# Optimization experiments

Hardware: AMD Instinct MI355X
Metric: run time of the kernel (lower is better)

The kernel has to match this reference:

```python
import jax, jax.numpy as jnp
import numpy as np

V, E, HID, L = 32000, 2048, 8192, 4
H, KV, DK, DH = 16, 4, 128, 128
SEQ, WINDOW = 2048, 1024
EPS = 1e-5


def rms_norm(x):
    return x * jax.lax.rsqrt(jnp.mean(x * x, axis=-1, keepdims=True) + EPS)


def rope_buffers(seq_len, key_size):
    half = key_size // 2
    offset = jnp.arange(key_size) % half
    scales = jnp.power(10000.0, -2.0 / key_size * offset.astype(jnp.float32))
    angles = jnp.arange(seq_len, dtype=jnp.float32)[:, None] * scales[None, :]  # [S, DK]
    cos = jnp.cos(angles)
    sin = jnp.sin(angles)
    sin = sin.at[:, :half].multiply(-1.0)
    return cos, sin


def rotate(f, cos, sin):
    # f: [B, heads, S, DK]; cos/sin: [S, DK]
    half = DK // 2
    swapped = jnp.concatenate([f[..., half:], f[..., :half]], axis=-1)
    return cos * f + sin * swapped


def sliding_window_attention(q, k, v, window):
    # q: [B,H,S,DK], k: [B,KV,S,DK], v: [B,KV,S,DH]; GQA broadcast
    B, _, S, _ = q.shape
    G = H // KV
    qg = q.reshape(B, KV, G, S, DK)
    scores = jnp.einsum('bkgqd,bkjd->bkgqj', qg, k) / jnp.sqrt(jnp.asarray(DK, q.dtype))
    i = jnp.arange(S)[:, None]
    j = jnp.arange(S)[None, :]
    mask = (j <= i) & (i - j < window)
    scores = jnp.where(mask, scores, jnp.asarray(-1e9, scores.dtype))
    probs = jax.nn.softmax(scores, axis=-1)
    out = jnp.einsum('bkgqj,bkjd->bkgqd', probs, v)
    return out.reshape(B, H, S, DH)


def setup_inputs() -> dict:
    key = jax.random.key(0)
    ks = jax.random.split(key, 9)
    s = lambda k, shape, fan: jax.random.normal(k, shape, jnp.float32) / np.sqrt(fan)
    return {
        'tokens': jax.random.randint(ks[0], (1, SEQ), 0, V),
        'table': jax.random.normal(ks[1], (V, E), jnp.float32) * 0.02,
        'wq': s(ks[2], (L, E, H * DK), E),
        'wk': s(ks[3], (L, E, KV * DK), E),
        'wv': s(ks[4], (L, E, KV * DH), E),
        'wo': s(ks[5], (L, H * DH, E), H * DH),
        'w_up': s(ks[6], (L, E, 2 * HID), E),
        'w_down': s(ks[7], (L, HID, E), HID),
        'w_vocab': s(ks[8], (E, V), E),
    }


def reference(tokens, table, wq, wk, wv, wo, w_up, w_down, w_vocab):
    B, S = tokens.shape
    table = table.at[0].set(0.0)  # forward zeroes row 0 each call
    cos, sin = rope_buffers(S, DK)
    x = table[tokens]  # [B, S, E]
    for l in range(L):
        # --- self attention ---
        n = rms_norm(x)
        q = (n @ wq[l]).reshape(B, S, H, DK).transpose(0, 2, 1, 3)
        k = (n @ wk[l]).reshape(B, S, KV, DK).transpose(0, 2, 1, 3)
        v = (n @ wv[l]).reshape(B, S, KV, DH).transpose(0, 2, 1, 3)
        q = rotate(q, cos, sin)
        k = rotate(k, cos, sin)
        attn = sliding_window_attention(q, k, v, WINDOW)
        attn = attn.transpose(0, 2, 1, 3).reshape(B, S, H * DH)
        x = x + attn @ wo[l]
        # --- SwiGLU FFN ---
        n = rms_norm(x)
        gu = n @ w_up[l]
        gate, up = gu[..., :HID], gu[..., HID:]
        x = x + (up * jax.nn.silu(gate)) @ w_down[l]
    x = rms_norm(x)
    logits = x @ w_vocab  # [B, S, V]
    return logits
```

## Files before the change

### kernel.cpp

```cpp
#include <hip/hip_runtime.h>
#include <cstdint>

typedef unsigned short bf16u;
typedef __attribute__((ext_vector_type(8))) short short8;
typedef __attribute__((ext_vector_type(4))) short short4v;
typedef __attribute__((ext_vector_type(4))) float f32x4;

#define SEQ   2048
#define EMB   2048
#define NHEAD 16
#define NKV   4
#define DKH   128
#define HIDN  8192
#define NVOC  32000
#define NLAY  4
#define WIN   1024
#define QKV_N 3072

__device__ __forceinline__ bf16u f2bf(float f) {
  union { float f; uint32_t u; } v; v.f = f;
  uint32_t r = v.u + 0x7FFFu + ((v.u >> 16) & 1u);
  return (bf16u)(r >> 16);
}

__device__ __forceinline__ void gl2lds16(const void* g, void* l) {
  __builtin_amdgcn_global_load_lds(
      (const __attribute__((address_space(1))) void*)g,
      (__attribute__((address_space(3))) void*)l, 16, 0, 0);
}

__global__ __launch_bounds__(256) void embed_kernel(const int* __restrict__ tokens,
                                                    const float* __restrict__ table,
                                                    float* __restrict__ x) {
  int s = blockIdx.x;
  int tok = tokens[s];
  int i0 = threadIdx.x * 8;
  float4 a = {0,0,0,0}, b = {0,0,0,0};
  if (tok != 0) {
    const float* src = table + (size_t)tok * EMB;
    a = *(const float4*)(src + i0);
    b = *(const float4*)(src + i0 + 4);
  }
  *(float4*)(x + (size_t)s * EMB + i0) = a;
  *(float4*)(x + (size_t)s * EMB + i0 + 4) = b;
}

__global__ __launch_bounds__(256) void rmsnorm_kernel(const float* __restrict__ x,
                                                      bf16u* __restrict__ out) {
  int s = blockIdx.x;
  const float* row = x + (size_t)s * EMB;
  int i0 = threadIdx.x * 8;
  float4 a = *(const float4*)(row + i0);
  float4 b = *(const float4*)(row + i0 + 4);
  float ss = a.x*a.x + a.y*a.y + a.z*a.z + a.w*a.w
           + b.x*b.x + b.y*b.y + b.z*b.z + b.w*b.w;
  #pragma unroll
  for (int off = 1; off < 64; off <<= 1) ss += __shfl_xor(ss, off);
  __shared__ float red[4];
  if ((threadIdx.x & 63) == 0) red[threadIdx.x >> 6] = ss;
  __syncthreads();
  float scale = rsqrtf((red[0] + red[1] + red[2] + red[3]) * (1.0f / EMB) + 1e-5f);
  float v[8] = {a.x, a.y, a.z, a.w, b.x, b.y, b.z, b.w};
  short8 o;
  #pragma unroll
  for (int j = 0; j < 8; ++j) o[j] = (short)f2bf(v[j] * scale);
  *(short8*)(out + (size_t)s * EMB + i0) = o;
}

__global__ __launch_bounds__(256) void reduce4norm_kernel(float* __restrict__ x,
                                                          const float* __restrict__ p,
                                                          bf16u* __restrict__ nout) {
  int s = blockIdx.x;
  const size_t MN = (size_t)SEQ * EMB;
  size_t base = (size_t)s * EMB + threadIdx.x * 8;
  float v[8];
  #pragma unroll
  for (int h = 0; h < 2; ++h) {
    size_t i = base + h * 4;
    float4 a  = *(const float4*)(x + i);
    float4 b0 = *(const float4*)(p + i);
    float4 b1 = *(const float4*)(p + i + MN);
    float4 b2 = *(const float4*)(p + i + 2 * MN);
    float4 b3 = *(const float4*)(p + i + 3 * MN);
    v[h*4+0] = a.x + b0.x + b1.x + b2.x + b3.x;
    v[h*4+1] = a.y + b0.y + b1.y + b2.y + b3.y;
    v[h*4+2] = a.z + b0.z + b1.z + b2.z + b3.z;
    v[h*4+3] = a.w + b0.w + b1.w + b2.w + b3.w;
    *(float4*)(x + i) = make_float4(v[h*4+0], v[h*4+1], v[h*4+2], v[h*4+3]);
  }
  float ss = 0.0f;
  #pragma unroll
  for (int j = 0; j < 8; ++j) ss += v[j] * v[j];
  #pragma unroll
  for (int off = 1; off < 64; off <<= 1) ss += __shfl_xor(ss, off);
  __shared__ float red[4];
  if ((threadIdx.x & 63) == 0) red[threadIdx.x >> 6] = ss;
  __syncthreads();
  float scale = rsqrtf((red[0] + red[1] + red[2] + red[3]) * (1.0f / EMB) + 1e-5f);
  short8 o;
  #pragma unroll
  for (int j = 0; j < 8; ++j) o[j] = (short)f2bf(v[j] * scale);
  *(short8*)(nout + base) = o;
}

__global__ __launch_bounds__(256) void transp_kernel(const float* __restrict__ in,
                                                     bf16u* __restrict__ out,
                                                     int R, int C, int pairhalf) {
  __shared__ float tile[64][65];
  int c0 = blockIdx.x * 64, r0 = blockIdx.y * 64;
  int tx = threadIdx.x & 15, ty = threadIdx.x >> 4;
  #pragma unroll
  for (int i = 0; i < 4; ++i) {
    int r = ty + i * 16;
    float4 v = *(const float4*)(in + (size_t)(r0 + r) * C + c0 + tx * 4);
    tile[tx * 4 + 0][r] = v.x;
    tile[tx * 4 + 1][r] = v.y;
    tile[tx * 4 + 2][r] = v.z;
    tile[tx * 4 + 3][r] = v.w;
  }
  __syncthreads();
  int rx = threadIdx.x & 15, cy = threadIdx.x >> 4;
  #pragma unroll
  for (int i = 0; i < 4; ++i) {
    int c = c0 + cy + i * 16;
    int n = pairhalf ? (c < pairhalf ? 2 * c : 2 * (c - pairhalf) + 1) : c;
    short4v o;
    #pragma unroll
    for (int j = 0; j < 4; ++j) o[j] = (short)f2bf(tile[cy + i * 16][rx * 4 + j]);
    *(short4v*)(out + (size_t)n * R + r0 + rx * 4) = o;
  }
}

__global__ __launch_bounds__(256) void rope_kernel(const float* __restrict__ qkv,
                                                   bf16u* __restrict__ out, int col0) {
  int idx = blockIdx.x * 256 + threadIdx.x;
  int d = idx & 63;
  int s = (idx >> 6) & (SEQ - 1);
  int h = idx >> 17;
  const float* row = qkv + (size_t)s * QKV_N + col0 + h * DKH;
  float ang = (float)s * __powf(10000.0f, -(float)d * (1.0f / 64.0f));
  float si, c;
  sincosf(ang, &si, &c);
  float f0 = row[d], f1 = row[d + 64];
  bf16u* orow = out + ((size_t)h * SEQ + s) * DKH;
  orow[d]      = f2bf(c * f0 - si * f1);
  orow[d + 64] = f2bf(c * f1 + si * f0);
}

__global__ __launch_bounds__(256) void vconv_kernel(const float* __restrict__ qkv,
                                                    bf16u* __restrict__ vout) {
  int idx = blockIdx.x * 256 + threadIdx.x;
  int d = idx & 127;
  int kv = (idx >> 7) & 3;
  int s = idx >> 9;
  vout[((size_t)kv * SEQ + s) * DKH + d] = f2bf(qkv[(size_t)s * QKV_N + 2560 + kv * DKH + d]);
}

template <int MODE>
__global__ __launch_bounds__(256) void gemm_kernel(const bf16u* __restrict__ A,
                                                   const bf16u* __restrict__ Bt,
                                                   void* __restrict__ C,
                                                   int M, int N, int K) {
  __shared__ __align__(16) char lds[2][2][8192];

  int nx = gridDim.x, ny = gridDim.y;
  int nwg = nx * ny;
  int orig = blockIdx.y * nx + blockIdx.x;
  int q = nwg >> 3, r = nwg & 7;
  int xcd = orig & 7, loc = orig >> 3;
  int id = (xcd < r ? xcd * (q + 1) : r * (q + 1) + (xcd - r) * q) + loc;
  int bx = id / ny, by = id - bx * ny;
  int n0 = bx * 128, m0 = by * 128;

  int t = threadIdx.x;
  int w = t >> 6, l = t & 63;
  int wm = (w >> 1) * 64, wn = (w & 1) * 64;
  int l15 = l & 15, l4 = l >> 4;

  int srow = w * 16 + (l >> 2);
  int scol = (l & 3) * 8;

  f32x4 acc[4][4] = {};

  auto stage = [&](int buf, int k0) {
    #pragma unroll
    for (int i = 0; i < 2; ++i) {
      gl2lds16(A  + (size_t)(m0 + i * 64 + srow) * K + k0 + scol,
               &lds[buf][0][i * 4096 + w * 1024]);
      gl2lds16(Bt + (size_t)(n0 + i * 64 + srow) * K + k0 + scol,
               &lds[buf][1][i * 4096 + w * 1024]);
    }
  };

  auto compute = [&](int buf) {
    short8 af[4], bfr[4];
    #pragma unroll
    for (int i = 0; i < 4; ++i) {
      af[i]  = *(const short8*)(&lds[buf][0][((wm + i * 16 + l15) * 32 + l4 * 8) * 2]);
      bfr[i] = *(const short8*)(&lds[buf][1][((wn + i * 16 + l15) * 32 + l4 * 8) * 2]);
    }
    #pragma unroll
    for (int i = 0; i < 4; ++i)
      #pragma unroll
      for (int j = 0; j < 4; ++j)
        acc[i][j] = __builtin_amdgcn_mfma_f32_16x16x32_bf16(af[i], bfr[j], acc[i][j], 0, 0, 0);
  };

  int nt = K >> 5;
  int cur = 0;
  stage(0, 0);
  __syncthreads();
  for (int tt = 0; tt < nt; ++tt) {
    if (tt + 1 < nt) stage(cur ^ 1, (tt + 1) * 32);
    compute(cur);
    __syncthreads();
    cur ^= 1;
  }

  #pragma unroll
  for (int i = 0; i < 4; ++i)
    #pragma unroll
    for (int j = 0; j < 4; ++j) {
      int col = n0 + wn + j * 16 + l15;
      #pragma unroll
      for (int rr = 0; rr < 4; ++rr) {
        int row = m0 + wm + i * 16 + l4 * 4 + rr;
        float v = acc[i][j][rr];
        if (MODE == 0) {
          ((bf16u*)C)[(size_t)row * N + col] = f2bf(v);
        } else if (MODE == 1) {
          float* p = (float*)C + (size_t)row * N + col;
          *p += v;
        } else {
          ((float*)C)[(size_t)row * N + col] = v;
        }
      }
    }
}

__device__ __forceinline__ void stage_half(const bf16u* __restrict__ p, int ld,
                                           int row0, int k0, char* slotBase, int t) {
  int r  = t >> 3, c8 = t & 7;
  int cs = (c8 ^ (r & 7)) << 3;
  gl2lds16(p + (size_t)(row0 + r) * ld + k0 + cs, slotBase + t * 16);
  gl2lds16(p + (size_t)(row0 + 64 + r) * ld + k0 + cs, slotBase + 8192 + t * 16);
}

template<int KK>
__device__ __forceinline__ short8 read_frag(const char* slot, int row, int l4) {
  int kc = KK * 4 + l4;
  return *(const short8*)(slot + row * 128 + ((kc ^ (row & 7)) << 4));
}

template<int NH>
__device__ __forceinline__ void mfma_quad(f32x4 (&acc)[8][4], const short8 (&a)[8],
                                          short8 b0, short8 b1) {
  __builtin_amdgcn_s_setprio(1);
  #pragma unroll
  for (int mi = 0; mi < 8; ++mi) {
    acc[mi][NH * 2]     = __builtin_amdgcn_mfma_f32_16x16x32_bf16(a[mi], b0, acc[mi][NH * 2], 0, 0, 0);
    acc[mi][NH * 2 + 1] = __builtin_amdgcn_mfma_f32_16x16x32_bf16(a[mi], b1, acc[mi][NH * 2 + 1], 0, 0, 0);
  }
  __builtin_amdgcn_s_setprio(0);
}

template <int MODE>
__global__ __launch_bounds__(512) void gemm256_kernel(const bf16u* __restrict__ A,
                                                      const bf16u* __restrict__ Bt,
                                                      void* __restrict__ C,
                                                      int M, int N, int K, int ldk) {
  __shared__ __align__(16) char lds[131072];

  int koff = blockIdx.z * K;
  A  += koff;
  Bt += koff;
  float* Cz = (float*)C + (size_t)blockIdx.z * M * N;

  int nx = gridDim.x, ny = gridDim.y;
  int nwg = nx * ny;
  int orig = blockIdx.y * nx + blockIdx.x;
  int q8 = nwg >> 3, r8 = nwg & 7;
  int xcd = orig & 7, loc = orig >> 3;
  int id = (xcd < r8 ? xcd * (q8 + 1) : r8 * (q8 + 1) + (xcd - r8) * q8) + loc;
  int bx = id / ny, by = id - bx * ny;
  int n0 = bx * 256, m0 = by * 256;

  int t = threadIdx.x;
  int wid = t >> 6, lane = t & 63;
  int wr = wid >> 2, wc = wid & 3, bh = wc >> 1;
  int l15 = lane & 15, l4 = lane >> 4;

  char* AS0 = lds;              char* AS1 = lds + 16384;
  char* AS2 = lds + 32768;      char* AS3 = lds + 49152;
  char* BS0 = lds + 65536;      char* BS1 = lds + 81920;
  char* BS2 = lds + 98304;      char* BS3 = lds + 114688;

  const char* ASe = lds + wr * 16384;
  const char* ASo = ASe + 32768;
  const char* BSe = lds + 65536 + bh * 16384;
  const char* BSo = BSe + 32768;

  int brow = (wc & 1) * 64;

  f32x4 acc[8][4] = {};
  short8 a[8];
  short8 b0, b1;

  int NT = K >> 6;
  int NI = NT >> 1;

  stage_half(A,  ldk, m0,       0,  AS0, t);
  stage_half(A,  ldk, m0 + 128, 0,  AS1, t);
  stage_half(Bt, ldk, n0,       0,  BS0, t);
  stage_half(Bt, ldk, n0 + 128, 0,  BS1, t);
  stage_half(A,  ldk, m0,       64, AS2, t);
  asm volatile("s_waitcnt vmcnt(2)" ::: "memory");
  __builtin_amdgcn_s_barrier();
  __builtin_amdgcn_sched_barrier(0);

  for (int I = 0; I < NI; ++I) {
    int t0k = I * 128;
    int t1k = t0k + 64;
    bool notlast = (I + 1 < NI);

    #pragma unroll
    for (int mi = 0; mi < 8; ++mi) a[mi] = read_frag<0>(ASe, mi * 16 + l15, l4);
    b0 = read_frag<0>(BSe, brow + l15, l4);
    b1 = read_frag<0>(BSe, brow + 16 + l15, l4);
    stage_half(A, ldk, m0 + 128, t1k, AS3, t);
    __builtin_amdgcn_s_barrier();
    mfma_quad<0>(acc, a, b0, b1);
    __builtin_amdgcn_s_barrier();

    b0 = read_frag<0>(BSe, brow + 32 + l15, l4);
    b1 = read_frag<0>(BSe, brow + 48 + l15, l4);
    stage_half(Bt, ldk, n0, t1k, BS2, t);
    __builtin_amdgcn_s_barrier();
    mfma_quad<1>(acc, a, b0, b1);
    __builtin_amdgcn_s_barrier();

    #pragma unroll
    for (int mi = 0; mi < 8; ++mi) a[mi] = read_frag<1>(ASe, mi * 16 + l15, l4);
    b0 = read_frag<1>(BSe, brow + l15, l4);
    b1 = read_frag<1>(BSe, brow + 16 + l15, l4);
    stage_half(Bt, ldk, n0 + 128, t1k, BS3, t);
    __builtin_amdgcn_s_barrier();
    mfma_quad<0>(acc, a, b0, b1);
    __builtin_amdgcn_s_barrier();

    b0 = read_frag<1>(BSe, brow + 32 + l15, l4);
    b1 = read_frag<1>(BSe, brow + 48 + l15, l4);
    if (notlast) stage_half(A, ldk, m0, t0k + 128, AS0, t);
    if (notlast) { asm volatile("s_waitcnt vmcnt(2)" ::: "memory"); }
    else         { asm volatile("s_waitcnt vmcnt(0)" ::: "memory"); }
    __builtin_amdgcn_s_barrier();
    __builtin_amdgcn_sched_barrier(0);
    mfma_quad<1>(acc, a, b0, b1);
    __builtin_amdgcn_s_barrier();

    #pragma unroll
    for (int mi = 0; mi < 8; ++mi) a[mi] = read_frag<0>(ASo, mi * 16 + l15, l4);
    b0 = read_frag<0>(BSo, brow + l15, l4);
    b1 = read_frag<0>(BSo, brow + 16 + l15, l4);
    if (notlast) stage_half(A, ldk, m0 + 128, t0k + 128, AS1, t);
    __builtin_amdgcn_s_barrier();
    mfma_quad<0>(acc, a, b0, b1);
    __builtin_amdgcn_s_barrier();

    b0 = read_frag<0>(BSo, brow + 32 + l15, l4);
    b1 = read_frag<0>(BSo, brow + 48 + l15, l4);
    if (notlast) stage_half(Bt, ldk, n0, t0k + 128, BS0, t);
    __builtin_amdgcn_s_barrier();
    mfma_quad<1>(acc, a, b0, b1);
    __builtin_amdgcn_s_barrier();

    #pragma unroll
    for (int mi = 0; mi < 8; ++mi) a[mi] = read_frag<1>(ASo, mi * 16 + l15, l4);
    b0 = read_frag<1>(BSo, brow + l15, l4);
    b1 = read_frag<1>(BSo, brow + 16 + l15, l4);
    if (notlast) stage_half(Bt, ldk, n0 + 128, t0k + 128, BS1, t);
    __builtin_amdgcn_s_barrier();
    mfma_quad<0>(acc, a, b0, b1);
    __builtin_amdgcn_s_barrier();

    b0 = read_frag<1>(BSo, brow + 32 + l15, l4);
    b1 = read_frag<1>(BSo, brow + 48 + l15, l4);
    if (notlast) {
      stage_half(A, ldk, m0, t0k + 192, AS2, t);
      asm volatile("s_waitcnt vmcnt(2)" ::: "memory");
    }
    __builtin_amdgcn_s_barrier();
    __builtin_amdgcn_sched_barrier(0);
    mfma_quad<1>(acc, a, b0, b1);
    __builtin_amdgcn_s_barrier();
  }

  #pragma unroll
  for (int mi = 0; mi < 8; ++mi)
    #pragma unroll
    for (int ni = 0; ni < 4; ++ni) {
      int col = n0 + wc * 64 + ni * 16 + l15;
      #pragma unroll
      for (int rr = 0; rr < 4; ++rr) {
        int row = m0 + wr * 128 + mi * 16 + l4 * 4 + rr;
        float v = acc[mi][ni][rr];
        if (MODE == 3) {
          float pv = __shfl_xor(v, 1);
          if ((l15 & 1) == 0) {
            float hval = pv * (v / (1.0f + __expf(-v)));
            ((bf16u*)C)[(size_t)row * HIDN + (col >> 1)] = f2bf(hval);
          }
        } else if (MODE == 2) {
          Cz[(size_t)row * N + col] = v;
        } else if (MODE == 1) {
          float* p = (float*)C + (size_t)row * N + col;
          *p += v;
        } else {
          ((bf16u*)C)[(size_t)row * N + col] = f2bf(v);
        }
      }
    }
}

__global__ __launch_bounds__(512) void attn_kernel(const bf16u* __restrict__ q_bf,
                                                   const bf16u* __restrict__ k_bf,
                                                   const bf16u* __restrict__ v_bf,
                                                   bf16u* __restrict__ attn_out) {
  int h = blockIdx.y;
  int q0 = blockIdx.x * 128;
  int kvh = h >> 2;
  const bf16u* Kp = k_bf + (size_t)kvh * SEQ * DKH;
  const bf16u* Vp = v_bf + (size_t)kvh * SEQ * DKH;

  __shared__ __align__(16) char  Klds[64 * 128 * 2];
  __shared__ __align__(16) bf16u Vlds[128][72];
  __shared__ __align__(16) bf16u Plds[8][16][72];

  int t = threadIdx.x, wave = t >> 6, lane = t & 63;
  int l15 = lane & 15, l4 = lane >> 4;
  int qrow0 = q0 + wave * 16;

  short8 qf[4];
  #pragma unroll
  for (int ks = 0; ks < 4; ++ks)
    qf[ks] = *(const short8*)(q_bf + ((size_t)h * SEQ + qrow0 + l15) * DKH + ks * 32 + l4 * 8);

  f32x4 o[8] = {};
  float m[4], lsum[4];
  #pragma unroll
  for (int r = 0; r < 4; ++r) { m[r] = -INFINITY; lsum[r] = 0.0f; }

  int vkey = t & 63, vd0 = (t >> 6) * 16;

  int jstart = q0 >= WIN ? ((q0 - (WIN - 1)) & ~63) : 0;

  for (int j0 = jstart; j0 < q0 + 128; j0 += 64) {
    __syncthreads();
    #pragma unroll
    for (int i = 0; i < 2; ++i) {
      int c = t + i * 512;
      int key = c >> 4, cc = c & 15;
      int off = key * 256 + cc * 16; off ^= (key & 7) << 4;
      *(short8*)(Klds + off) = *(const short8*)(Kp + (size_t)(j0 + key) * DKH + cc * 8);
    }
    {
      const bf16u* src = Vp + (size_t)(j0 + vkey) * DKH + vd0;
      short8 v0 = *(const short8*)(src);
      short8 v1 = *(const short8*)(src + 8);
      #pragma unroll
      for (int i = 0; i < 8; ++i) Vlds[vd0 + i][vkey] = (bf16u)(unsigned short)v0[i];
      #pragma unroll
      for (int i = 0; i < 8; ++i) Vlds[vd0 + 8 + i][vkey] = (bf16u)(unsigned short)v1[i];
    }
    __syncthreads();

    f32x4 sacc[4] = {};
    #pragma unroll
    for (int nt = 0; nt < 4; ++nt) {
      int key = nt * 16 + l15;
      #pragma unroll
      for (int ks = 0; ks < 4; ++ks) {
        int off = key * 256 + ks * 64 + l4 * 16; off ^= (key & 7) << 4;
        short8 kf = *(short8*)(Klds + off);
        sacc[nt] = __builtin_amdgcn_mfma_f32_16x16x32_bf16(qf[ks], kf, sacc[nt], 0, 0, 0);
      }
    }

    float sv[4][4];
    #pragma unroll
    for (int nt = 0; nt < 4; ++nt) {
      int jk = j0 + nt * 16 + l15;
      #pragma unroll
      for (int r = 0; r < 4; ++r) {
        int iq = qrow0 + l4 * 4 + r;
        float s = sacc[nt][r] * 0.08838834764831845f;
        bool valid = (jk <= iq) && (iq - jk < WIN);
        sv[nt][r] = valid ? s : -1e9f;
      }
    }

    float mxr[4];
    #pragma unroll
    for (int r = 0; r < 4; ++r) {
      float mx = fmaxf(fmaxf(sv[0][r], sv[1][r]), fmaxf(sv[2][r], sv[3][r]));
      #pragma unroll
      for (int off = 1; off < 16; off <<= 1) mx = fmaxf(mx, __shfl_xor(mx, off));
      mxr[r] = mx;
    }

    bool grow = (mxr[0] > m[0] + 8.0f) || (mxr[1] > m[1] + 8.0f) ||
                (mxr[2] > m[2] + 8.0f) || (mxr[3] > m[3] + 8.0f);
    if (__any(grow)) {
      #pragma unroll
      for (int r = 0; r < 4; ++r) {
        float mn = fmaxf(m[r], mxr[r]);
        float alpha = __expf(m[r] - mn);
        m[r] = mn;
        lsum[r] *= alpha;
        #pragma unroll
        for (int d = 0; d < 8; ++d) o[d][r] *= alpha;
      }
    }

    float p[4][4];
    #pragma unroll
    for (int r = 0; r < 4; ++r) {
      float ps = 0.0f;
      #pragma unroll
      for (int nt = 0; nt < 4; ++nt) { p[nt][r] = __expf(sv[nt][r] - m[r]); ps += p[nt][r]; }
      #pragma unroll
      for (int off = 1; off < 16; off <<= 1) ps += __shfl_xor(ps, off);
      lsum[r] += ps;
    }

    #pragma unroll
    for (int nt = 0; nt < 4; ++nt)
      #pragma unroll
      for (int r = 0; r < 4; ++r)
        Plds[wave][l4 * 4 + r][nt * 16 + l15] = f2bf(p[nt][r]);

    #pragma unroll
    for (int kk = 0; kk < 2; ++kk) {
      short8 pf = *(short8*)(&Plds[wave][l15][kk * 32 + l4 * 8]);
      #pragma unroll
      for (int d = 0; d < 8; ++d) {
        short8 vf = *(short8*)(&Vlds[d * 16 + l15][kk * 32 + l4 * 8]);
        o[d] = __builtin_amdgcn_mfma_f32_16x16x32_bf16(pf, vf, o[d], 0, 0, 0);
      }
    }
  }

  #pragma unroll
  for (int d = 0; d < 8; ++d)
    #pragma unroll
    for (int r = 0; r < 4; ++r) {
      int row = qrow0 + l4 * 4 + r;
      attn_out[(size_t)row * (NHEAD * DKH) + h * DKH + d * 16 + l15] = f2bf(o[d][r] / lsum[r]);
    }
}

extern "C" void kernel_launch(void* const* d_in, const int* in_sizes, int n_in,
                              void* d_out, int out_size, void* d_ws, size_t ws_size,
                              hipStream_t stream) {
  const int*   tokens  = (const int*)d_in[0];
  const float* table   = (const float*)d_in[1];
  const float* wq      = (const float*)d_in[2];
  const float* wk      = (const float*)d_in[3];
  const float* wv      = (const float*)d_in[4];
  const float* wo      = (const float*)d_in[5];
  const float* w_up    = (const float*)d_in[6];
  const float* w_down  = (const float*)d_in[7];
  const float* w_vocab = (const float*)d_in[8];
  float* out = (float*)d_out;

  char* base = (char*)d_ws;
  size_t o = 0;
  auto alloc = [&](size_t bytes) { size_t r = o; o += (bytes + 255) & ~(size_t)255; return r; };
  size_t o_x     = alloc((size_t)SEQ * EMB * 4);
  size_t o_nbf   = alloc((size_t)SEQ * EMB * 2);
  size_t o_qkvw  = alloc((size_t)QKV_N * EMB * 2);
  size_t o_wot   = alloc((size_t)EMB * EMB * 2);
  size_t o_wupt  = alloc((size_t)2 * HIDN * EMB * 2);
  size_t o_wdnt  = alloc((size_t)EMB * HIDN * 2);
  size_t o_qkvf  = alloc((size_t)SEQ * QKV_N * 4);
  size_t o_qbf   = alloc((size_t)NHEAD * SEQ * DKH * 2);
  size_t o_kbf   = alloc((size_t)NKV * SEQ * DKH * 2);
  size_t o_vbf   = alloc((size_t)NKV * SEQ * DKH * 2);
  size_t o_attn  = alloc((size_t)SEQ * EMB * 2);
  size_t o_big   = alloc((size_t)SEQ * 2 * HIDN * 4);
  size_t o_hbf   = alloc((size_t)SEQ * HIDN * 2);

  float* x      = (float*)(base + o_x);
  bf16u* n_bf   = (bf16u*)(base + o_nbf);
  bf16u* qkvw_t = (bf16u*)(base + o_qkvw);
  bf16u* wo_t   = (bf16u*)(base + o_wot);
  bf16u* wup_t  = (bf16u*)(base + o_wupt);
  bf16u* wdn_t  = (bf16u*)(base + o_wdnt);
  float* qkv_f  = (float*)(base + o_qkvf);
  bf16u* q_bf   = (bf16u*)(base + o_qbf);
  bf16u* k_bf   = (bf16u*)(base + o_kbf);
  bf16u* v_bf   = (bf16u*)(base + o_vbf);
  bf16u* attn_b = (bf16u*)(base + o_attn);
  float* part   = (float*)(base + o_big);
  bf16u* h_bf   = (bf16u*)(base + o_hbf);
  bf16u* wvoc_t = (bf16u*)(base + o_big);

  embed_kernel<<<SEQ, 256, 0, stream>>>(tokens, table, x);
  rmsnorm_kernel<<<SEQ, 256, 0, stream>>>(x, n_bf);

  for (int l = 0; l < NLAY; ++l) {
    transp_kernel<<<dim3(EMB / 64, EMB / 64), 256, 0, stream>>>(
        wq + (size_t)l * EMB * EMB, qkvw_t, EMB, EMB, 0);
    transp_kernel<<<dim3(512 / 64, EMB / 64), 256, 0, stream>>>(
        wk + (size_t)l * EMB * 512, qkvw_t + (size_t)2048 * EMB, EMB, 512, 0);
    transp_kernel<<<dim3(512 / 64, EMB / 64), 256, 0, stream>>>(
        wv + (size_t)l * EMB * 512, qkvw_t + (size_t)2560 * EMB, EMB, 512, 0);
    transp_kernel<<<dim3(EMB / 64, EMB / 64), 256, 0, stream>>>(
        wo + (size_t)l * EMB * EMB, wo_t, EMB, EMB, 0);
    transp_kernel<<<dim3(2 * HIDN / 64, EMB / 64), 256, 0, stream>>>(
        w_up + (size_t)l * EMB * 2 * HIDN, wup_t, EMB, 2 * HIDN, HIDN);
    transp_kernel<<<dim3(EMB / 64, HIDN / 64), 256, 0, stream>>>(
        w_down + (size_t)l * HIDN * EMB, wdn_t, HIDN, EMB, 0);

    gemm_kernel<2><<<dim3(QKV_N / 128, SEQ / 128), 256, 0, stream>>>(
        n_bf, qkvw_t, qkv_f, SEQ, QKV_N, EMB);

    rope_kernel<<<NHEAD * SEQ * 64 / 256, 256, 0, stream>>>(qkv_f, q_bf, 0);
    rope_kernel<<<NKV * SEQ * 64 / 256, 256, 0, stream>>>(qkv_f, k_bf, 2048);
    vconv_kernel<<<NKV * SEQ * 128 / 256, 256, 0, stream>>>(qkv_f, v_bf);

    attn_kernel<<<dim3(SEQ / 128, NHEAD), 512, 0, stream>>>(q_bf, k_bf, v_bf, attn_b);

    gemm_kernel<1><<<dim3(EMB / 128, SEQ / 128), 256, 0, stream>>>(
        attn_b, wo_t, x, SEQ, EMB, EMB);

    rmsnorm_kernel<<<SEQ, 256, 0, stream>>>(x, n_bf);
    gemm256_kernel<3><<<dim3(2 * HIDN / 256, SEQ / 256), 512, 0, stream>>>(
        n_bf, wup_t, h_bf, SEQ, 2 * HIDN, EMB, EMB);
    gemm256_kernel<2><<<dim3(EMB / 256, SEQ / 256, 4), 512, 0, stream>>>(
        h_bf, wdn_t, part, SEQ, EMB, 2048, HIDN);
    reduce4norm_kernel<<<SEQ, 256, 0, stream>>>(x, part, n_bf);
  }

  transp_kernel<<<dim3(NVOC / 64, EMB / 64), 256, 0, stream>>>(w_vocab, wvoc_t, EMB, NVOC, 0);
  gemm256_kernel<2><<<dim3(NVOC / 256, SEQ / 256), 512, 0, stream>>>(
      n_bf, wvoc_t, out, SEQ, NVOC, EMB, EMB);
}
```

Measured before the change: 2.467 ms.

## Batch weight transposes across layers and keep QKV output in bf16

Weight transposes for all four layers now run up front as batched launches (one grid z-slice per layer) into per-layer buffers, replacing six launches per layer with six launches in total. The QKV GEMM writes bf16 directly instead of fp32, and a single rope launch now handles both Q and K heads. The separate V conversion kernel is removed: attention reads V straight from the strided bf16 QKV buffer. This cuts launch count and memory traffic, but the workspace grows to hold every layer's transposed weights, and the strided V reads may coalesce less well.

```diff
diff --git a/kernel.cpp b/kernel.cpp
--- a/kernel.cpp
+++ b/kernel.cpp
@@ -21,6 +21,10 @@
   union { float f; uint32_t u; } v; v.f = f;
   uint32_t r = v.u + 0x7FFFu + ((v.u >> 16) & 1u);
   return (bf16u)(r >> 16);
+}
+__device__ __forceinline__ float bf2f(bf16u b) {
+  union { uint32_t u; float f; } v; v.u = ((uint32_t)b) << 16;
+  return v.f;
 }
 
 __device__ __forceinline__ void gl2lds16(const void* g, void* l) {
@@ -105,8 +109,11 @@
 
 __global__ __launch_bounds__(256) void transp_kernel(const float* __restrict__ in,
                                                      bf16u* __restrict__ out,
-                                                     int R, int C, int pairhalf) {
+                                                     int R, int C, int pairhalf,
+                                                     size_t ostride) {
   __shared__ float tile[64][65];
+  in  += (size_t)blockIdx.z * R * C;
+  out += (size_t)blockIdx.z * ostride;
   int c0 = blockIdx.x * 64, r0 = blockIdx.y * 64;
   int tx = threadIdx.x & 15, ty = threadIdx.x >> 4;
   #pragma unroll
@@ -131,29 +138,23 @@
   }
 }
 
-__global__ __launch_bounds__(256) void rope_kernel(const float* __restrict__ qkv,
-                                                   bf16u* __restrict__ out, int col0) {
+__global__ __launch_bounds__(256) void rope_kernel(const bf16u* __restrict__ qkv,
+                                                   bf16u* __restrict__ q_bf,
+                                                   bf16u* __restrict__ k_bf) {
   int idx = blockIdx.x * 256 + threadIdx.x;
   int d = idx & 63;
   int s = (idx >> 6) & (SEQ - 1);
   int h = idx >> 17;
-  const float* row = qkv + (size_t)s * QKV_N + col0 + h * DKH;
+  int col0 = (h < NHEAD) ? h * DKH : 2048 + (h - NHEAD) * DKH;
+  const bf16u* row = qkv + (size_t)s * QKV_N + col0;
   float ang = (float)s * __powf(10000.0f, -(float)d * (1.0f / 64.0f));
   float si, c;
   sincosf(ang, &si, &c);
-  float f0 = row[d], f1 = row[d + 64];
-  bf16u* orow = out + ((size_t)h * SEQ + s) * DKH;
+  float f0 = bf2f(row[d]), f1 = bf2f(row[d + 64]);
+  bf16u* orow = (h < NHEAD) ? q_bf + ((size_t)h * SEQ + s) * DKH
+                            : k_bf + ((size_t)(h - NHEAD) * SEQ + s) * DKH;
   orow[d]      = f2bf(c * f0 - si * f1);
   orow[d + 64] = f2bf(c * f1 + si * f0);
-}
-
-__global__ __launch_bounds__(256) void vconv_kernel(const float* __restrict__ qkv,
-                                                    bf16u* __restrict__ vout) {
-  int idx = blockIdx.x * 256 + threadIdx.x;
-  int d = idx & 127;
-  int kv = (idx >> 7) & 3;
-  int s = idx >> 9;
-  vout[((size_t)kv * SEQ + s) * DKH + d] = f2bf(qkv[(size_t)s * QKV_N + 2560 + kv * DKH + d]);
 }
 
 template <int MODE>
@@ -424,13 +425,13 @@
 
 __global__ __launch_bounds__(512) void attn_kernel(const bf16u* __restrict__ q_bf,
                                                    const bf16u* __restrict__ k_bf,
-                                                   const bf16u* __restrict__ v_bf,
+                                                   const bf16u* __restrict__ qkv_bf,
                                                    bf16u* __restrict__ attn_out) {
   int h = blockIdx.y;
   int q0 = blockIdx.x * 128;
   int kvh = h >> 2;
   const bf16u* Kp = k_bf + (size_t)kvh * SEQ * DKH;
-  const bf16u* Vp = v_bf + (size_t)kvh * SEQ * DKH;
+  const bf16u* Vp = qkv_bf + 2560 + kvh * DKH;
 
   __shared__ __align__(16) char  Klds[64 * 128 * 2];
   __shared__ __align__(16) bf16u Vlds[128][72];
@@ -464,7 +465,7 @@
       *(short8*)(Klds + off) = *(const short8*)(Kp + (size_t)(j0 + key) * DKH + cc * 8);
     }
     {
-      const bf16u* src = Vp + (size_t)(j0 + vkey) * DKH + vd0;
+      const bf16u* src = Vp + (size_t)(j0 + vkey) * QKV_N + vd0;
       short8 v0 = *(const short8*)(src);
       short8 v1 = *(const short8*)(src + 8);
       #pragma unroll
@@ -578,14 +579,13 @@
   auto alloc = [&](size_t bytes) { size_t r = o; o += (bytes + 255) & ~(size_t)255; return r; };
   size_t o_x     = alloc((size_t)SEQ * EMB * 4);
   size_t o_nbf   = alloc((size_t)SEQ * EMB * 2);
-  size_t o_qkvw  = alloc((size_t)QKV_N * EMB * 2);
-  size_t o_wot   = alloc((size_t)EMB * EMB * 2);
-  size_t o_wupt  = alloc((size_t)2 * HIDN * EMB * 2);
-  size_t o_wdnt  = alloc((size_t)EMB * HIDN * 2);
-  size_t o_qkvf  = alloc((size_t)SEQ * QKV_N * 4);
+  size_t o_qkvw  = alloc((size_t)NLAY * QKV_N * EMB * 2);
+  size_t o_wot   = alloc((size_t)NLAY * EMB * EMB * 2);
+  size_t o_wupt  = alloc((size_t)NLAY * 2 * HIDN * EMB * 2);
+  size_t o_wdnt  = alloc((size_t)NLAY * EMB * HIDN * 2);
+  size_t o_qkvbf = alloc((size_t)SEQ * QKV_N * 2);
   size_t o_qbf   = alloc((size_t)NHEAD * SEQ * DKH * 2);
   size_t o_kbf   = alloc((size_t)NKV * SEQ * DKH * 2);
-  size_t o_vbf   = alloc((size_t)NKV * SEQ * DKH * 2);
   size_t o_attn  = alloc((size_t)SEQ * EMB * 2);
   size_t o_big   = alloc((size_t)SEQ * 2 * HIDN * 4);
   size_t o_hbf   = alloc((size_t)SEQ * HIDN * 2);
@@ -596,53 +596,53 @@
   bf16u* wo_t   = (bf16u*)(base + o_wot);
   bf16u* wup_t  = (bf16u*)(base + o_wupt);
   bf16u* wdn_t  = (bf16u*)(base + o_wdnt);
-  float* qkv_f  = (float*)(base + o_qkvf);
+  bf16u* qkv_bf = (bf16u*)(base + o_qkvbf);
   bf16u* q_bf   = (bf16u*)(base + o_qbf);
   bf16u* k_bf   = (bf16u*)(base + o_kbf);
-  bf16u* v_bf   = (bf16u*)(base + o_vbf);
   bf16u* attn_b = (bf16u*)(base + o_attn);
   float* part   = (float*)(base + o_big);
   bf16u* h_bf   = (bf16u*)(base + o_hbf);
   bf16u* wvoc_t = (bf16u*)(base + o_big);
 
+  const size_t QKVW = (size_t)QKV_N * EMB;
+
+  transp_kernel<<<dim3(EMB / 64, EMB / 64, NLAY), 256, 0, stream>>>(
+      wq, qkvw_t, EMB, EMB, 0, QKVW);
+  transp_kernel<<<dim3(512 / 64, EMB / 64, NLAY), 256, 0, stream>>>(
+      wk, qkvw_t + (size_t)2048 * EMB, EMB, 512, 0, QKVW);
+  transp_kernel<<<dim3(512 / 64, EMB / 64, NLAY), 256, 0, stream>>>(
+      wv, qkvw_t + (size_t)2560 * EMB, EMB, 512, 0, QKVW);
+  transp_kernel<<<dim3(EMB / 64, EMB / 64, NLAY), 256, 0, stream>>>(
+      wo, wo_t, EMB, EMB, 0, (size_t)EMB * EMB);
+  transp_kernel<<<dim3(2 * HIDN / 64, EMB / 64, NLAY), 256, 0, stream>>>(
+      w_up, wup_t, EMB, 2 * HIDN, HIDN, (size_t)2 * HIDN * EMB);
+  transp_kernel<<<dim3(EMB / 64, HIDN / 64, NLAY), 256, 0, stream>>>(
+      w_down, wdn_t, HIDN, EMB, 0, (size_t)EMB * HIDN);
+
   embed_kernel<<<SEQ, 256, 0, stream>>>(tokens, table, x);
   rmsnorm_kernel<<<SEQ, 256, 0, stream>>>(x, n_bf);
 
   for (int l = 0; l < NLAY; ++l) {
-    transp_kernel<<<dim3(EMB / 64, EMB / 64), 256, 0, stream>>>(
-        wq + (size_t)l * EMB * EMB, qkvw_t, EMB, EMB, 0);
-    transp_kernel<<<dim3(512 / 64, EMB / 64), 256, 0, stream>>>(
-        wk + (size_t)l * EMB * 512, qkvw_t + (size_t)2048 * EMB, EMB, 512, 0);
-    transp_kernel<<<dim3(512 / 64, EMB / 64), 256, 0, stream>>>(
-        wv + (size_t)l * EMB * 512, qkvw_t + (size_t)2560 * EMB, EMB, 512, 0);
-    transp_kernel<<<dim3(EMB / 64, EMB / 64), 256, 0, stream>>>(
-        wo + (size_t)l * EMB * EMB, wo_t, EMB, EMB, 0);
-    transp_kernel<<<dim3(2 * HIDN / 64, EMB / 64), 256, 0, stream>>>(
-        w_up + (size_t)l * EMB * 2 * HIDN, wup_t, EMB, 2 * HIDN, HIDN);
-    transp_kernel<<<dim3(EMB / 64, HIDN / 64), 256, 0, stream>>>(
-        w_down + (size_t)l * HIDN * EMB, wdn_t, HIDN, EMB, 0);
-
-    gemm_kernel<2><<<dim3(QKV_N / 128, SEQ / 128), 256, 0, stream>>>(
-        n_bf, qkvw_t, qkv_f, SEQ, QKV_N, EMB);
-
-    rope_kernel<<<NHEAD * SEQ * 64 / 256, 256, 0, stream>>>(qkv_f, q_bf, 0);
-    rope_kernel<<<NKV * SEQ * 64 / 256, 256, 0, stream>>>(qkv_f, k_bf, 2048);
-    vconv_kernel<<<NKV * SEQ * 128 / 256, 256, 0, stream>>>(qkv_f, v_bf);
-
-    attn_kernel<<<dim3(SEQ / 128, NHEAD), 512, 0, stream>>>(q_bf, k_bf, v_bf, attn_b);
+    gemm_kernel<0><<<dim3(QKV_N / 128, SEQ / 128), 256, 0, stream>>>(
+        n_bf, qkvw_t + (size_t)l * QKVW, qkv_bf, SEQ, QKV_N, EMB);
+
+    rope_kernel<<<(NHEAD + NKV) * SEQ * 64 / 256, 256, 0, stream>>>(qkv_bf, q_bf, k_bf);
+
+    attn_kernel<<<dim3(SEQ / 128, NHEAD), 512, 0, stream>>>(q_bf, k_bf, qkv_bf, attn_b);
 
     gemm_kernel<1><<<dim3(EMB / 128, SEQ / 128), 256, 0, stream>>>(
-        attn_b, wo_t, x, SEQ, EMB, EMB);
+        attn_b, wo_t + (size_t)l * EMB * EMB, x, SEQ, EMB, EMB);
 
     rmsnorm_kernel<<<SEQ, 256, 0, stream>>>(x, n_bf);
     gemm256_kernel<3><<<dim3(2 * HIDN / 256, SEQ / 256), 512, 0, stream>>>(
-        n_bf, wup_t, h_bf, SEQ, 2 * HIDN, EMB, EMB);
+        n_bf, wup_t + (size_t)l * 2 * HIDN * EMB, h_bf, SEQ, 2 * HIDN, EMB, EMB);
     gemm256_kernel<2><<<dim3(EMB / 256, SEQ / 256, 4), 512, 0, stream>>>(
-        h_bf, wdn_t, part, SEQ, EMB, 2048, HIDN);
+        h_bf, wdn_t + (size_t)l * EMB * HIDN, part, SEQ, EMB, 2048, HIDN);
     reduce4norm_kernel<<<SEQ, 256, 0, stream>>>(x, part, n_bf);
   }
 
-  transp_kernel<<<dim3(NVOC / 64, EMB / 64), 256, 0, stream>>>(w_vocab, wvoc_t, EMB, NVOC, 0);
+  transp_kernel<<<dim3(NVOC / 64, EMB / 64, 1), 256, 0, stream>>>(
+      w_vocab, wvoc_t, EMB, NVOC, 0, 0);
   gemm256_kernel<2><<<dim3(NVOC / 256, SEQ / 256), 512, 0, stream>>>(
       n_bf, wvoc_t, out, SEQ, NVOC, EMB, EMB);
 }
```

After: 2.349 ms. 4.7% less time.
